# Optimization experiments

Hardware: AMD Instinct MI355X
Metric: run time of the kernel (lower is better)

## Reference

```python
import jax, jax.numpy as jnp
import numpy as np

B, P, C_IN, C = 2, 100000, 23, 64
H, W = 512, 512
S = H * W  # num voxels per batch element
EPS_BN1, EPS_BN2 = 1e-5, 1e-3


def setup_inputs() -> dict:
    key = jax.random.key(0)
    ks = jax.random.split(key, 16)
    valid = jax.random.uniform(ks[0], (B, P)) > 0.1
    inp = {
        "points_xyz": jax.random.normal(ks[1], (B, P, 3), jnp.float32),
        "points_feature": jax.random.normal(ks[2], (B, P, C_IN), jnp.float32),
        "points_mask": valid.astype(jnp.float32),
        "indices": jax.random.randint(ks[3], (B, P), 0, S, jnp.int32),
        "paddings": (1 - valid.astype(jnp.int32)),
        "voxel_xyz": jax.random.uniform(ks[4], (B, P, 3), jnp.float32) * 511.0,
        # PointNet linear (bias=False) + BatchNorm1d params (eval-style stats)
        "w_pn": jax.random.normal(ks[5], (C_IN, C), jnp.float32) * 0.1,
        "bn1_gamma": jax.random.uniform(ks[6], (C,), jnp.float32, 0.5, 1.5),
        "bn1_beta": jax.random.normal(ks[7], (C,), jnp.float32) * 0.1,
        "bn1_mean": jax.random.normal(ks[8], (C,), jnp.float32) * 0.1,
        "bn1_var": jax.random.uniform(ks[9], (C,), jnp.float32, 0.5, 1.5),
        # res1: Conv2d 1x1 (bias=False) + BatchNorm2d
        "conv_w": jax.random.normal(ks[10], (C, C), jnp.float32) * 0.05,  # [out,in]
        "bn2_gamma": jax.random.uniform(ks[11], (C,), jnp.float32, 0.5, 1.5),
        "bn2_beta": jax.random.normal(ks[12], (C,), jnp.float32) * 0.1,
        "bn2_mean": jax.random.normal(ks[13], (C,), jnp.float32) * 0.1,
        "bn2_var": jax.random.uniform(ks[14], (C,), jnp.float32, 0.5, 1.5),
    }
    return inp


def reference(points_xyz, points_feature, points_mask, indices, paddings, voxel_xyz,
              w_pn, bn1_gamma, bn1_beta, bn1_mean, bn1_var,
              conv_w, bn2_gamma, bn2_beta, bn2_mean, bn2_var):
    # ---- PointNet: Linear -> BN -> ReLU -> mask ----
    x = jnp.einsum("bpi,io->bpo", points_feature, w_pn)
    x = (x - bn1_mean) * jax.lax.rsqrt(bn1_var + EPS_BN1) * bn1_gamma + bn1_beta
    x = jax.nn.relu(x) * points_mask[..., None]  # [B,P,C]

    # ---- batched unsorted segment max (padded points -> dummy segment) ----
    valid = paddings == 0
    batch_off = jnp.arange(B, dtype=jnp.int32)[:, None] * S
    flat_ids = jnp.where(valid, indices + batch_off, B * S).reshape(-1)
    voxels = jax.ops.segment_max(x.reshape(B * P, C), flat_ids,
                                 num_segments=B * S + 1)[: B * S]
    voxels = jnp.where(jnp.isneginf(voxels), 0.0, voxels)  # empty voxels -> 0
    v = voxels.reshape(B, H, W, C)

    # ---- res1: 1x1 conv + BN + ReLU (NHWC layout) ----
    v = jnp.einsum("bhwc,oc->bhwo", v, conv_w)
    v = (v - bn2_mean) * jax.lax.rsqrt(bn2_var + EPS_BN2) * bn2_gamma + bn2_beta
    v = jax.nn.relu(v)

    # torch: voxels[B,C,H,W].permute(0,3,2,1) -> [B,W,H,C]; x indexes W, y indexes H
    im = jnp.transpose(v, (0, 2, 1, 3))  # [B,W,H,C]

    # ---- bilinear gather at voxel_xyz[..., :2] ----
    xq = voxel_xyz[..., 0]
    yq = voxel_xyz[..., 1]
    x0 = jnp.clip(jnp.floor(xq).astype(jnp.int32), 0, W - 1)
    x1 = jnp.clip(x0 + 1, 0, W - 1)
    y0 = jnp.clip(jnp.floor(yq).astype(jnp.int32), 0, H - 1)
    y1 = jnp.clip(y0 + 1, 0, H - 1)
    bidx = jnp.arange(B, dtype=jnp.int32)[:, None]
    Ia = im[bidx, x0, y0]
    Ib = im[bidx, x0, y1]
    Ic = im[bidx, x1, y0]
    Id = im[bidx, x1, y1]
    x0f, x1f = x0.astype(xq.dtype), x1.astype(xq.dtype)
    y0f, y1f = y0.astype(yq.dtype), y1.astype(yq.dtype)
    wa = (x1f - xq) * (y1f - yq)
    wb = (x1f - xq) * (yq - y0f)
    wc = (xq - x0f) * (y1f - yq)
    wd = (xq - x0f) * (yq - y0f)
    points_out = (wa[..., None] * Ia + wb[..., None] * Ib
                  + wc[..., None] * Ic + wd[..., None] * Id)  # [B,P,C]
    return points_out
```

## Files before the change

### kernel.cpp

```cpp
#include <hip/hip_runtime.h>
#include <hip/hip_bf16.h>

#define B_ 2
#define P_ 100000
#define CIN_ 23
#define C_ 64
#define H_ 512
#define W_ 512
#define S_ (H_*W_)
#define NPT_ (B_*P_)
#define NVOX_ (B_*S_)

typedef __attribute__((ext_vector_type(8))) short short8;
typedef __attribute__((ext_vector_type(4))) float f32x4;
typedef __attribute__((ext_vector_type(4))) int i32x4;
typedef __attribute__((ext_vector_type(4), aligned(4))) float f32x4u;

__device__ inline unsigned short f2bf(float f) {
    union { __hip_bfloat16 h; unsigned short u; } cv;
    cv.h = __float2bfloat16(f);
    return cv.u;
}
__device__ inline float bf2f(unsigned short u) {
    union { unsigned int i; float f; } cv;
    cv.i = ((unsigned int)u) << 16;
    return cv.f;
}
__device__ inline void bf2x(unsigned int u, float& lo, float& hi) {
    union { unsigned int i; float f; } a, b;
    a.i = u << 16;
    b.i = u & 0xffff0000u;
    lo = a.f; hi = b.f;
}

__global__ __launch_bounds__(256) void k_clear(int* __restrict__ cnt)
{
    int i = (blockIdx.x * 256 + threadIdx.x) * 4;
    if (i > NVOX_) return;
    *(i32x4*)(cnt + i) = (i32x4){0, 0, 0, 0};
}

__global__ __launch_bounds__(256) void k_hist(
    const int* __restrict__ indices,
    const int* __restrict__ paddings,
    int* __restrict__ cnt)
{
    int t4 = (blockIdx.x * 256 + threadIdx.x) * 4;
    if (t4 >= NPT_) return;
    i32x4 idx4 = *(const i32x4*)(indices + t4);
    i32x4 pad4 = *(const i32x4*)(paddings + t4);
    int vb = (t4 / P_) * S_;
    #pragma unroll
    for (int j = 0; j < 4; ++j)
        if (pad4[j] == 0) atomicAdd(&cnt[vb + idx4[j]], 1);
}

__global__ __launch_bounds__(256) void k_offsets(
    const int* __restrict__ cnt,
    int* __restrict__ cur,
    int* __restrict__ rid,
    int* __restrict__ off_c,
    int* __restrict__ cnt_c,
    int* __restrict__ gcursor,
    const float* __restrict__ conv_w,
    const float* __restrict__ w_pn,
    const float* __restrict__ g1, const float* __restrict__ b1,
    const float* __restrict__ m1, const float* __restrict__ v1,
    const float* __restrict__ g2, const float* __restrict__ b2,
    const float* __restrict__ m2, const float* __restrict__ v2,
    unsigned short* __restrict__ cwb,
    unsigned short* __restrict__ wpb,
    float* __restrict__ o1v,
    float* __restrict__ scv, float* __restrict__ shv)
{
    if (blockIdx.x >= 512) {
        int t = threadIdx.x;
        if (t < 64) {
            float s = g1[t] * rsqrtf(v1[t] + 1e-5f);
            o1v[t] = b1[t] - m1[t] * s;
            float s2 = g2[t] * rsqrtf(v2[t] + 1e-3f);
            scv[t] = s2;
            shv[t] = b2[t] - m2[t] * s2;
        }
        #pragma unroll
        for (int e = 0; e < 16; ++e) {
            int idx  = t * 16 + e;
            int f    = idx >> 9;
            int lane = (idx >> 3) & 63;
            int j    = idx & 7;
            int tq = f >> 1, ks = f & 1;
            int row = lane & 15, grp = lane >> 4;
            cwb[idx] = f2bf(conv_w[(tq * 16 + row) * 64 + ks * 32 + grp * 8 + j]);
        }
        #pragma unroll
        for (int e = 0; e < 8; ++e) {
            int idx  = t * 8 + e;
            int tq   = idx >> 9;
            int lane = (idx >> 3) & 63;
            int j    = idx & 7;
            int row = lane & 15, grp = lane >> 4;
            int n = tq * 16 + row;
            int k = grp * 8 + j;
            float s1n = g1[n] * rsqrtf(v1[n] + 1e-5f);
            wpb[idx] = (k < CIN_) ? f2bf(w_pn[k * C_ + n] * s1n) : 0;
        }
        return;
    }

    __shared__ int lds_c[256], lds_o[256];
    __shared__ int sbase_c, sbase_o;
    int tid  = threadIdx.x;
    int base = blockIdx.x * 1024 + tid * 4;
    i32x4 c = *(const i32x4*)(cnt + base);
    int o0 = c[0] > 0, o1 = c[1] > 0, o2 = c[2] > 0, o3 = c[3] > 0;
    int sc1 = c[0] + c[1], sc2 = sc1 + c[2], sc3 = sc2 + c[3];
    int so1 = o0 + o1,     so2 = so1 + o2,   so3 = so2 + o3;
    lds_c[tid] = sc3;
    lds_o[tid] = so3;
    __syncthreads();
    #pragma unroll
    for (int d = 1; d < 256; d <<= 1) {
        int vc = (tid >= d) ? lds_c[tid - d] : 0;
        int vo = (tid >= d) ? lds_o[tid - d] : 0;
        __syncthreads();
        if (tid >= d) { lds_c[tid] += vc; lds_o[tid] += vo; }
        __syncthreads();
    }
    if (tid == 0) {
        sbase_c = atomicAdd(&gcursor[0], lds_c[255]);
        sbase_o = atomicAdd(&gcursor[1], lds_o[255]);
    }
    __syncthreads();
    int oc = sbase_c + (tid == 0 ? 0 : lds_c[tid - 1]);
    int oo = sbase_o + (tid == 0 ? 0 : lds_o[tid - 1]);
    i32x4 e, ridv;
    e[0] = oc; e[1] = oc + c[0]; e[2] = oc + sc1; e[3] = oc + sc2;
    ridv[0] = o0 ? oo            : -1;
    ridv[1] = o1 ? oo + so1 - o1 : -1;
    ridv[2] = o2 ? oo + so2 - o2 : -1;
    ridv[3] = o3 ? oo + so3 - o3 : -1;
    *(i32x4*)(cur + base) = e;
    *(i32x4*)(rid + base) = ridv;
    #pragma unroll
    for (int i = 0; i < 4; ++i) {
        if (ridv[i] >= 0) {
            off_c[ridv[i]] = e[i];
            cnt_c[ridv[i]] = c[i];
        }
    }
}

__global__ __launch_bounds__(256) void k_ptid(
    const int* __restrict__ indices,
    const int* __restrict__ paddings,
    int* __restrict__ cur,
    int* __restrict__ ptid)
{
    int pt = blockIdx.x * 256 + threadIdx.x;
    if (pt >= NPT_) return;
    if (paddings[pt] != 0) return;
    int v = (pt / P_) * S_ + indices[pt];
    int slot = atomicAdd(&cur[v], 1);
    ptid[slot] = pt;
}

__global__ __launch_bounds__(256) void k_redconv(
    const float* __restrict__ feat,
    const int* __restrict__ ptid,
    const int* __restrict__ off_c,
    const int* __restrict__ cnt_c,
    const int* __restrict__ gcursor,
    const unsigned short* __restrict__ wpb,
    const float* __restrict__ o1v,
    const unsigned short* __restrict__ cwb,
    const float* __restrict__ scv, const float* __restrict__ shv,
    unsigned short* __restrict__ grid_c)
{
    __shared__ unsigned short lds[4][16][64];

    int lane = threadIdx.x & 63;
    int wv   = threadIdx.x >> 6;
    int wid  = (blockIdx.x * 256 + threadIdx.x) >> 6;
    int r0   = wid * 16;
    int nocc = gcursor[1];
    if (r0 >= nocc) return;

    int col = lane & 15;
    int grp = lane >> 4;

    int rA    = r0 + col;
    bool livA = rA < nocc;
    int ciA   = livA ? cnt_c[rA] : 0;
    int oiA   = livA ? off_c[rA] : 0;

    int ci4[4];
    #pragma unroll
    for (int r = 0; r < 4; ++r) ci4[r] = __shfl(ciA, grp * 4 + r);

    short8 bz[4];
    #pragma unroll
    for (int t = 0; t < 4; ++t)
        bz[t] = *(const short8*)(wpb + ((size_t)t * 64 + lane) * 8);

    f32x4 mx[4];
    #pragma unroll
    for (int t = 0; t < 4; ++t) mx[t] = (f32x4){-1e30f, -1e30f, -1e30f, -1e30f};

    for (int j = 0; ; ++j) {
        if (!__any(j < ciA)) break;
        int jj = j < ciA ? j : 0;
        int pt = ptid[oiA + jj];
        const float* f = feat + (size_t)pt * CIN_;
        short8 a = (short8){0,0,0,0,0,0,0,0};
        if (grp < 3) {
            f32x4u v0 = *(const f32x4u*)(f + grp * 8);
            f32x4u v1 = *(const f32x4u*)(f + grp * 8 + 4);
            #pragma unroll
            for (int jx = 0; jx < 4; ++jx) {
                int k0 = grp * 8 + jx;
                int k1 = k0 + 4;
                a[jx]     = (short)(k0 < CIN_ ? f2bf(v0[jx]) : 0);
                a[jx + 4] = (short)(k1 < CIN_ ? f2bf(v1[jx]) : 0);
            }
        }
        #pragma unroll
        for (int t = 0; t < 4; ++t) {
            f32x4 zt = __builtin_amdgcn_mfma_f32_16x16x32_bf16(
                a, bz[t], (f32x4){0.f, 0.f, 0.f, 0.f}, 0, 0, 0);
            #pragma unroll
            for (int r = 0; r < 4; ++r)
                if (j < ci4[r]) mx[t][r] = fmaxf(mx[t][r], zt[r]);
        }
    }

    #pragma unroll
    for (int t = 0; t < 4; ++t) {
        float o1 = o1v[t * 16 + col];
        #pragma unroll
        for (int r = 0; r < 4; ++r) {
            int row = grp * 4 + r;
            float val = fmaxf(mx[t][r] + o1, 0.f);
            lds[wv][row][(t * 16 + col) ^ ((row & 7) << 3)] = f2bf(val);
        }
    }

    short8 a2[2];
    #pragma unroll
    for (int ks = 0; ks < 2; ++ks)
        a2[ks] = *(const short8*)&lds[wv][col][(ks * 32 + grp * 8) ^ ((col & 7) << 3)];

    short8 bfrag[4][2];
    #pragma unroll
    for (int t = 0; t < 4; ++t)
        #pragma unroll
        for (int ks = 0; ks < 2; ++ks)
            bfrag[t][ks] = *(const short8*)(cwb + ((size_t)(t * 2 + ks) * 64 + lane) * 8);

    f32x4 acc[4];
    #pragma unroll
    for (int t = 0; t < 4; ++t) acc[t] = (f32x4){0.f, 0.f, 0.f, 0.f};
    #pragma unroll
    for (int t = 0; t < 4; ++t) {
        acc[t] = __builtin_amdgcn_mfma_f32_16x16x32_bf16(a2[0], bfrag[t][0], acc[t], 0, 0, 0);
        acc[t] = __builtin_amdgcn_mfma_f32_16x16x32_bf16(a2[1], bfrag[t][1], acc[t], 0, 0, 0);
    }

    float sc[4], sh[4];
    #pragma unroll
    for (int t = 0; t < 4; ++t) {
        int n = t * 16 + col;
        sc[t] = scv[n];
        sh[t] = shv[n];
    }
    #pragma unroll
    for (int rq = 0; rq < 4; ++rq) {
        int rr = r0 + grp * 4 + rq;
        if (rr < nocc) {
            unsigned short* op = grid_c + (size_t)rr * C_;
            #pragma unroll
            for (int t = 0; t < 4; ++t) {
                float val = fmaxf(acc[t][rq] * sc[t] + sh[t], 0.f);
                op[t * 16 + col] = f2bf(val);
            }
        }
    }
}

__global__ __launch_bounds__(256) void k_gather32(
    const unsigned short* __restrict__ grid_c,
    const int* __restrict__ rid,
    const float* __restrict__ vxyz,
    const float* __restrict__ shv,
    float* __restrict__ out)
{
    int lane = threadIdx.x & 63;
    int q    = lane >> 4;
    int ch   = (lane & 15) * 4;
    int gw   = (blockIdx.x * 256 + threadIdx.x) >> 6;
    int p0   = gw * 32;
    if (p0 >= NPT_) return;

    f32x4 cstv = *(const f32x4*)(shv + ch);
    #pragma unroll
    for (int j = 0; j < 4; ++j) cstv[j] = fmaxf(cstv[j], 0.f);

    const unsigned short* gc = grid_c + ch;

    #pragma unroll
    for (int it = 0; it < 8; ++it) {
        int pt = p0 + it * 4 + q;
        int b  = pt / P_;
        float xq = vxyz[(size_t)pt * 3 + 0];
        float yq = vxyz[(size_t)pt * 3 + 1];
        int x0 = (int)floorf(xq); x0 = min(max(x0, 0), W_ - 1);
        int x1 = min(x0 + 1, W_ - 1);
        int y0 = (int)floorf(yq); y0 = min(max(y0, 0), H_ - 1);
        int y1 = min(y0 + 1, H_ - 1);
        float x0f = (float)x0, x1f = (float)x1, y0f = (float)y0, y1f = (float)y1;
        float wa = (x1f - xq) * (y1f - yq);
        float wb = (x1f - xq) * (yq - y0f);
        float wc = (xq - x0f) * (y1f - yq);
        float wd = (xq - x0f) * (yq - y0f);

        int ia = y0 * W_ + x0, ib = y1 * W_ + x0, ic = y0 * W_ + x1, id = y1 * W_ + x1;
        const int* rb = rid + (size_t)b * S_;

        int ra = rb[ia], rbn = rb[ib], rc = rb[ic], rd = rb[id];
        uint2 Ra = *(const uint2*)(gc + (size_t)max(ra,  0) * C_);
        uint2 Rb = *(const uint2*)(gc + (size_t)max(rbn, 0) * C_);
        uint2 Rc = *(const uint2*)(gc + (size_t)max(rc,  0) * C_);
        uint2 Rd = *(const uint2*)(gc + (size_t)max(rd,  0) * C_);

        float A0,A1,A2,A3, B0,B1,B2,B3, C0,C1,C2,C3, D0,D1,D2,D3;
        bf2x(Ra.x, A0, A1); bf2x(Ra.y, A2, A3);
        bf2x(Rb.x, B0, B1); bf2x(Rb.y, B2, B3);
        bf2x(Rc.x, C0, C1); bf2x(Rc.y, C2, C3);
        bf2x(Rd.x, D0, D1); bf2x(Rd.y, D2, D3);

        bool oa = ra >= 0, ob = rbn >= 0, oc = rc >= 0, od = rd >= 0;
        f32x4 res;
        res[0] = wa * (oa ? A0 : cstv[0]) + wb * (ob ? B0 : cstv[0])
               + wc * (oc ? C0 : cstv[0]) + wd * (od ? D0 : cstv[0]);
        res[1] = wa * (oa ? A1 : cstv[1]) + wb * (ob ? B1 : cstv[1])
               + wc * (oc ? C1 : cstv[1]) + wd * (od ? D1 : cstv[1]);
        res[2] = wa * (oa ? A2 : cstv[2]) + wb * (ob ? B2 : cstv[2])
               + wc * (oc ? C2 : cstv[2]) + wd * (od ? D2 : cstv[2]);
        res[3] = wa * (oa ? A3 : cstv[3]) + wb * (ob ? B3 : cstv[3])
               + wc * (oc ? C3 : cstv[3]) + wd * (od ? D3 : cstv[3]);

        *(f32x4*)(out + (size_t)pt * C_ + ch) = res;
    }
}

extern "C" void kernel_launch(void* const* d_in, const int* in_sizes, int n_in,
                              void* d_out, int out_size, void* d_ws, size_t ws_size,
                              hipStream_t stream)
{
    const float* feat     = (const float*)d_in[1];
    const int*   indices  = (const int*)d_in[3];
    const int*   paddings = (const int*)d_in[4];
    const float* vxyz     = (const float*)d_in[5];
    const float* w_pn     = (const float*)d_in[6];
    const float* g1       = (const float*)d_in[7];
    const float* b1       = (const float*)d_in[8];
    const float* m1       = (const float*)d_in[9];
    const float* v1       = (const float*)d_in[10];
    const float* cw       = (const float*)d_in[11];
    const float* g2       = (const float*)d_in[12];
    const float* b2       = (const float*)d_in[13];
    const float* m2       = (const float*)d_in[14];
    const float* v2       = (const float*)d_in[15];

    char* p = (char*)d_ws;
    unsigned short* grid_c = (unsigned short*)p;  p += (size_t)NPT_ * C_ * 2;
    int* cnt   = (int*)p;  p += (size_t)NVOX_ * 4;
    int* gcur  = (int*)p;  p += 16;
    int* cur   = (int*)p;  p += (size_t)NVOX_ * 4;
    int* rid   = (int*)p;  p += (size_t)NVOX_ * 4;
    int* off_c = (int*)p;  p += (size_t)NPT_ * 4;
    int* cnt_c = (int*)p;  p += (size_t)NPT_ * 4;
    int* ptid  = (int*)p;  p += (size_t)NPT_ * 4;
    unsigned short* cwb = (unsigned short*)p;  p += 8 * 64 * 8 * 2;
    unsigned short* wpb = (unsigned short*)p;  p += 4 * 64 * 8 * 2;
    float* o1v = (float*)p;  p += 64 * 4;
    float* scv = (float*)p;  p += 64 * 4;
    float* shv = (float*)p;

    k_clear<<<513, 256, 0, stream>>>(cnt);

    k_hist<<<196, 256, 0, stream>>>(indices, paddings, cnt);

    k_offsets<<<513, 256, 0, stream>>>(cnt, cur, rid, off_c, cnt_c, gcur,
        cw, w_pn, g1, b1, m1, v1, g2, b2, m2, v2,
        cwb, wpb, o1v, scv, shv);

    k_ptid<<<(NPT_ + 255) / 256, 256, 0, stream>>>(indices, paddings, cur, ptid);

    k_redconv<<<3125, 256, 0, stream>>>(feat, ptid, off_c, cnt_c, gcur,
        wpb, o1v, cwb, scv, shv, grid_c);

    k_gather32<<<1563, 256, 0, stream>>>(grid_c, rid, vxyz, shv, (float*)d_out);
}
```

Before: 81.50 us.

## Partition occupied voxels into single-point and multi-point lists for reduction

The compaction scan now keeps two counters, one for voxels holding exactly one point and one for voxels holding several. Single-point voxels are packed from the front of the compacted array and multi-point voxels from the back. The reduce+conv kernel assigns whole waves to one class. Single-point waves skip the cnt_c load and the divergent max loop and run one MFMA pass, while multi-point waves keep the loop without being stalled by mixed row counts. This adds a third scan array and atomic, and relies on the new gcursor[2] slot being zeroed.

```diff
diff --git a/kernel.cpp b/kernel.cpp
--- a/kernel.cpp
+++ b/kernel.cpp
@@ -107,38 +107,49 @@
         return;
     }
 
-    __shared__ int lds_c[256], lds_o[256];
-    __shared__ int sbase_c, sbase_o;
+    __shared__ int lds_c[256], lds_a[256], lds_b[256];
+    __shared__ int sbase_c, sbase_a, sbase_b;
     int tid  = threadIdx.x;
     int base = blockIdx.x * 1024 + tid * 4;
     i32x4 c = *(const i32x4*)(cnt + base);
-    int o0 = c[0] > 0, o1 = c[1] > 0, o2 = c[2] > 0, o3 = c[3] > 0;
+    int a0 = c[0] == 1, a1 = c[1] == 1, a2 = c[2] == 1, a3 = c[3] == 1;
+    int b0 = c[0] >= 2, b1x = c[1] >= 2, b2x = c[2] >= 2, b3 = c[3] >= 2;
     int sc1 = c[0] + c[1], sc2 = sc1 + c[2], sc3 = sc2 + c[3];
-    int so1 = o0 + o1,     so2 = so1 + o2,   so3 = so2 + o3;
+    int sa1 = a0 + a1,     sa2 = sa1 + a2,   sa3 = sa2 + a3;
+    int sb1 = b0 + b1x,    sb2 = sb1 + b2x,  sb3 = sb2 + b3;
     lds_c[tid] = sc3;
-    lds_o[tid] = so3;
+    lds_a[tid] = sa3;
+    lds_b[tid] = sb3;
     __syncthreads();
     #pragma unroll
     for (int d = 1; d < 256; d <<= 1) {
         int vc = (tid >= d) ? lds_c[tid - d] : 0;
-        int vo = (tid >= d) ? lds_o[tid - d] : 0;
+        int va = (tid >= d) ? lds_a[tid - d] : 0;
+        int vb = (tid >= d) ? lds_b[tid - d] : 0;
         __syncthreads();
-        if (tid >= d) { lds_c[tid] += vc; lds_o[tid] += vo; }
+        if (tid >= d) { lds_c[tid] += vc; lds_a[tid] += va; lds_b[tid] += vb; }
         __syncthreads();
     }
     if (tid == 0) {
         sbase_c = atomicAdd(&gcursor[0], lds_c[255]);
-        sbase_o = atomicAdd(&gcursor[1], lds_o[255]);
+        sbase_a = atomicAdd(&gcursor[1], lds_a[255]);
+        sbase_b = atomicAdd(&gcursor[2], lds_b[255]);
     }
     __syncthreads();
     int oc = sbase_c + (tid == 0 ? 0 : lds_c[tid - 1]);
-    int oo = sbase_o + (tid == 0 ? 0 : lds_o[tid - 1]);
+    int oa = sbase_a + (tid == 0 ? 0 : lds_a[tid - 1]);
+    int ob = sbase_b + (tid == 0 ? 0 : lds_b[tid - 1]);
     i32x4 e, ridv;
     e[0] = oc; e[1] = oc + c[0]; e[2] = oc + sc1; e[3] = oc + sc2;
-    ridv[0] = o0 ? oo            : -1;
-    ridv[1] = o1 ? oo + so1 - o1 : -1;
-    ridv[2] = o2 ? oo + so2 - o2 : -1;
-    ridv[3] = o3 ? oo + so3 - o3 : -1;
+    int pa[4] = {0, sa1 - a1, sa2 - a2, sa3 - a3};
+    int pb[4] = {0, sb1 - b1x, sb2 - b2x, sb3 - b3};
+    #pragma unroll
+    for (int i = 0; i < 4; ++i) {
+        int ci = c[i];
+        ridv[i] = ci == 1 ? (oa + pa[i])
+                : ci >= 2 ? (NPT_ - 1 - (ob + pb[i]))
+                : -1;
+    }
     *(i32x4*)(cur + base) = e;
     *(i32x4*)(rid + base) = ridv;
     #pragma unroll
@@ -181,17 +192,23 @@
     int lane = threadIdx.x & 63;
     int wv   = threadIdx.x >> 6;
     int wid  = (blockIdx.x * 256 + threadIdx.x) >> 6;
-    int r0   = wid * 16;
-    int nocc = gcursor[1];
-    if (r0 >= nocc) return;
+
+    int nA = gcursor[1];
+    int nB = gcursor[2];
+    int wA = (nA + 15) >> 4;
+    int wB = (nB + 15) >> 4;
+    if (wid >= wA + wB) return;
+    bool isA = wid < wA;
+    int r0   = isA ? wid * 16 : (NPT_ - nB + (wid - wA) * 16);
+    int rtop = isA ? nA : NPT_;
 
     int col = lane & 15;
     int grp = lane >> 4;
 
     int rA    = r0 + col;
-    bool livA = rA < nocc;
-    int ciA   = livA ? cnt_c[rA] : 0;
+    bool livA = rA < rtop;
     int oiA   = livA ? off_c[rA] : 0;
+    int ciA   = isA ? (livA ? 1 : 0) : (livA ? cnt_c[rA] : 0);
 
     int ci4[4];
     #pragma unroll
@@ -206,10 +223,8 @@
     #pragma unroll
     for (int t = 0; t < 4; ++t) mx[t] = (f32x4){-1e30f, -1e30f, -1e30f, -1e30f};
 
-    for (int j = 0; ; ++j) {
-        if (!__any(j < ciA)) break;
-        int jj = j < ciA ? j : 0;
-        int pt = ptid[oiA + jj];
+    if (isA) {
+        int pt = ptid[oiA];
         const float* f = feat + (size_t)pt * CIN_;
         short8 a = (short8){0,0,0,0,0,0,0,0};
         if (grp < 3) {
@@ -229,7 +244,34 @@
                 a, bz[t], (f32x4){0.f, 0.f, 0.f, 0.f}, 0, 0, 0);
             #pragma unroll
             for (int r = 0; r < 4; ++r)
-                if (j < ci4[r]) mx[t][r] = fmaxf(mx[t][r], zt[r]);
+                if (ci4[r] > 0) mx[t][r] = zt[r];
+        }
+    } else {
+        for (int j = 0; ; ++j) {
+            if (!__any(j < ciA)) break;
+            int jj = j < ciA ? j : 0;
+            int pt = ptid[oiA + jj];
+            const float* f = feat + (size_t)pt * CIN_;
+            short8 a = (short8){0,0,0,0,0,0,0,0};
+            if (grp < 3) {
+                f32x4u v0 = *(const f32x4u*)(f + grp * 8);
+                f32x4u v1 = *(const f32x4u*)(f + grp * 8 + 4);
+                #pragma unroll
+                for (int jx = 0; jx < 4; ++jx) {
+                    int k0 = grp * 8 + jx;
+                    int k1 = k0 + 4;
+                    a[jx]     = (short)(k0 < CIN_ ? f2bf(v0[jx]) : 0);
+                    a[jx + 4] = (short)(k1 < CIN_ ? f2bf(v1[jx]) : 0);
+                }
+            }
+            #pragma unroll
+            for (int t = 0; t < 4; ++t) {
+                f32x4 zt = __builtin_amdgcn_mfma_f32_16x16x32_bf16(
+                    a, bz[t], (f32x4){0.f, 0.f, 0.f, 0.f}, 0, 0, 0);
+                #pragma unroll
+                for (int r = 0; r < 4; ++r)
+                    if (j < ci4[r]) mx[t][r] = fmaxf(mx[t][r], zt[r]);
+            }
         }
     }
 
@@ -275,7 +317,7 @@
     #pragma unroll
     for (int rq = 0; rq < 4; ++rq) {
         int rr = r0 + grp * 4 + rq;
-        if (rr < nocc) {
+        if (rr < rtop) {
             unsigned short* op = grid_c + (size_t)rr * C_;
             #pragma unroll
             for (int t = 0; t < 4; ++t) {
```

Result: slower. 85.91 us (+5.4%).
